# Optimization experiments

Hardware: AMD Instinct MI355X
Metric: run time of the kernel (lower is better)

Reference implementation:

```python
import jax, jax.numpy as jnp
import numpy as np

ALPHA = 0.1
BETA = 0.3
MARGIN = 2.0


def setup_inputs() -> dict:
    key = jax.random.key(0)
    k1, k2 = jax.random.split(key)
    prediction = jax.random.normal(k1, (8, 2048, 512), dtype=jnp.float32)
    target_seg = jax.random.randint(k2, (8, 2048), 0, 16, dtype=jnp.int64)
    return {"prediction": prediction, "target_seg": target_seg}


def _pairwise_sqdist(x):
    # x: [n, L, d] -> squared Euclidean distances [n, L, L] via a GEMM
    sq = jnp.sum(x * x, axis=-1)  # [n, L]
    inner = jnp.einsum('nld,nmd->nlm', x, x)  # [n, L, L]
    d2 = sq[:, :, None] + sq[:, None, :] - 2.0 * inner
    return jnp.maximum(d2, 0.0)


def _safe_sqrt(d2):
    # sqrt with zero (not NaN) gradient at 0, matching torch.cdist behavior
    pos = d2 > 0
    return jnp.where(pos, jnp.sqrt(jnp.where(pos, d2, 1.0)), 0.0)


def reference(prediction, target_seg):
    # y[i,j,k] = 1 if target_seg[i,j] == target_seg[i,k]
    y = (target_seg[:, :, None] == target_seg[:, None, :]).astype(prediction.dtype)
    d2 = _pairwise_sqdist(prediction)
    dist = _safe_sqrt(d2)
    hinge = jnp.maximum(MARGIN - dist, 0.0)
    loss = ALPHA * y * d2 + BETA * (1.0 - y) * hinge * hinge
    return jnp.mean(loss)
```

## Files before the change

### kernel.cpp

```cpp
#include <hip/hip_runtime.h>
#include <math.h>

#define L      2048
#define DDIM   512
#define NBATCH 8
#define BM     128
#define BN     128
#define BK     64
#define NKT    (DDIM / BK)
#define NTILE  (L / BM)
#define NPAIR  (NTILE * (NTILE + 1) / 2)
#define TOTAL_BLOCKS (NBATCH * NPAIR)

#define ALPHA  0.1f
#define BETA   0.3f
#define MARGIN 2.0f

typedef _Float16 f16x8 __attribute__((ext_vector_type(8)));
typedef __attribute__((ext_vector_type(16))) float f32x16;

#define TILE_SH 8192
#define BUFSZ   16384

#define GLOAD_LDS16(g, l) __builtin_amdgcn_global_load_lds(              \
    (const __attribute__((address_space(1))) unsigned int*)(g),          \
    (__attribute__((address_space(3))) unsigned int*)(l), 16, 0, 0)

__global__ __launch_bounds__(256) void conv_kernel(const float* __restrict__ pred,
                                                   _Float16* __restrict__ h,
                                                   float* __restrict__ sq) {
    int w    = threadIdx.x >> 6;
    int lane = threadIdx.x & 63;
    int row  = blockIdx.x * 4 + w;
    const float* p = pred + (size_t)row * DDIM + lane * 8;
    float4 v0 = *(const float4*)(p);
    float4 v1 = *(const float4*)(p + 4);
    float vals[8] = {v0.x, v0.y, v0.z, v0.w, v1.x, v1.y, v1.z, v1.w};
    f16x8 hv;
    float s = 0.0f;
    #pragma unroll
    for (int i = 0; i < 8; ++i) {
        float x = vals[i];
        s = fmaf(x, x, s);
        hv[i] = (_Float16)x;
    }
    *(f16x8*)(h + (size_t)row * DDIM + lane * 8) = hv;
    #pragma unroll
    for (int off = 32; off > 0; off >>= 1) s += __shfl_down(s, off);
    if (lane == 0) sq[row] = s;
}

__global__ __launch_bounds__(256, 2) void loss_kernel(
        const _Float16* __restrict__ h,
        const int*   __restrict__ seg,
        const float* __restrict__ sq,
        double*      __restrict__ partials) {
    __shared__ _Float16 smem[2 * BUFSZ];

    int bid = blockIdx.x;
    int n = bid & 7;
    int p = bid >> 3;
    int tj = 0;
    while (true) {
        int rl2 = NTILE - tj;
        if (p < rl2) break;
        p -= rl2;
        ++tj;
    }
    int tk = tj + p;
    int j0 = tj * BM, k0 = tk * BN;

    int t    = threadIdx.x;
    int w    = t >> 6;
    int lane = t & 63;
    int wr   = w >> 1, wc = w & 1;
    int l31  = lane & 31;
    int hsel = lane >> 5;

    const _Float16* baseH = h + (size_t)n * L * DDIM;

    int rl8 = lane >> 3;
    int lc  = (lane & 7) ^ rl8;
    const _Float16* srcAbase = baseH + (size_t)(j0 + rl8) * DDIM + lc * 8;
    const _Float16* srcBbase = baseH + (size_t)(k0 + rl8) * DDIM + lc * 8;

    f32x16 acc[2][2];
    #pragma unroll
    for (int m = 0; m < 2; ++m)
        #pragma unroll
        for (int nn = 0; nn < 2; ++nn)
            #pragma unroll
            for (int r = 0; r < 16; ++r) acc[m][nn][r] = 0.0f;

    #define STAGE(kt, b)                                                      \
    {                                                                         \
        _Float16* _A = smem + (b) * BUFSZ;                                    \
        _Float16* _B = _A + TILE_SH;                                          \
        _Pragma("unroll")                                                     \
        for (int q = 0; q < 4; ++q) {                                         \
            int inst = w * 4 + q;                                             \
            GLOAD_LDS16(srcAbase + (size_t)(inst * 8) * DDIM + (kt) * BK,     \
                        _A + inst * 512);                                     \
            GLOAD_LDS16(srcBbase + (size_t)(inst * 8) * DDIM + (kt) * BK,     \
                        _B + inst * 512);                                     \
        }                                                                     \
    }

    STAGE(0, 0);
    asm volatile("s_waitcnt vmcnt(0)" ::: "memory");
    __builtin_amdgcn_s_barrier();

    #pragma unroll
    for (int kt = 0; kt < NKT; ++kt) {
        const int cur = kt & 1;
        if (kt + 1 < NKT) STAGE(kt + 1, cur ^ 1);

        const _Float16* A = smem + cur * BUFSZ;
        const _Float16* B = A + TILE_SH;

        #pragma unroll
        for (int ks = 0; ks < 4; ++ks) {
            int c = ks * 2 + hsel;
            f16x8 af[2], bf[2];
            #pragma unroll
            for (int m = 0; m < 2; ++m) {
                int R = wr * 64 + m * 32 + l31;
                af[m] = *(const f16x8*)&A[R * 64 + ((c ^ (R & 7)) << 3)];
            }
            #pragma unroll
            for (int nn = 0; nn < 2; ++nn) {
                int R = wc * 64 + nn * 32 + l31;
                bf[nn] = *(const f16x8*)&B[R * 64 + ((c ^ (R & 7)) << 3)];
            }
            __builtin_amdgcn_s_setprio(1);
            #pragma unroll
            for (int m = 0; m < 2; ++m)
                #pragma unroll
                for (int nn = 0; nn < 2; ++nn)
                    acc[m][nn] = __builtin_amdgcn_mfma_f32_32x32x16_f16(
                        af[m], bf[nn], acc[m][nn], 0, 0, 0);
            __builtin_amdgcn_s_setprio(0);
        }

        asm volatile("s_waitcnt vmcnt(0)" ::: "memory");
        __builtin_amdgcn_s_barrier();
    }

    const int*   segb = seg + n * L;
    const float* sqb  = sq + n * L;

    float lsum = 0.0f;
    #pragma unroll
    for (int nn = 0; nn < 2; ++nn) {
        int k = k0 + wc * 64 + nn * 32 + l31;
        float sqk = sqb[k];
        int   sgk = segb[k];
        #pragma unroll
        for (int m = 0; m < 2; ++m)
            #pragma unroll
            for (int r = 0; r < 16; ++r) {
                int j = j0 + wr * 64 + m * 32 + (r & 3) + 8 * (r >> 2) + 4 * hsel;
                float inner = acc[m][nn][r];
                float d2 = fmaxf(sqb[j] + sqk - 2.0f * inner, 0.0f);
                float v;
                if (segb[j] == sgk) {
                    v = ALPHA * d2;
                } else {
                    float dist = sqrtf(d2);
                    float hg = fmaxf(MARGIN - dist, 0.0f);
                    v = BETA * hg * hg;
                }
                lsum += v;
            }
    }

    double wgt = (tj == tk) ? 1.0 : 2.0;
    __syncthreads();
    double* red = (double*)smem;
    red[t] = (double)lsum * wgt;
    __syncthreads();
    #pragma unroll
    for (int s = 128; s > 0; s >>= 1) {
        if (t < s) red[t] += red[t + s];
        __syncthreads();
    }
    if (t == 0) partials[blockIdx.x] = red[0];
}

__global__ __launch_bounds__(256) void reduce_kernel(const double* __restrict__ partials,
                                                     float* __restrict__ out,
                                                     int nPart, double invCount) {
    __shared__ double red[256];
    int t = threadIdx.x;
    double s = 0.0;
    for (int i = t; i < nPart; i += 256) s += partials[i];
    red[t] = s;
    __syncthreads();
    #pragma unroll
    for (int k = 128; k > 0; k >>= 1) {
        if (t < k) red[t] += red[t + k];
        __syncthreads();
    }
    if (t == 0) out[0] = (float)(red[0] * invCount);
}

extern "C" void kernel_launch(void* const* d_in, const int* in_sizes, int n_in,
                              void* d_out, int out_size, void* d_ws, size_t ws_size,
                              hipStream_t stream) {
    const float* pred = (const float*)d_in[0];
    const int*   seg  = (const int*)d_in[1];
    float* out = (float*)d_out;

    const size_t HALF = (size_t)NBATCH * L * DDIM;
    _Float16* h        = (_Float16*)d_ws;
    float*    sq       = (float*)(h + HALF);
    double*   partials = (double*)(sq + NBATCH * L);

    conv_kernel<<<NBATCH * L / 4, 256, 0, stream>>>(pred, h, sq);
    loss_kernel<<<TOTAL_BLOCKS, 256, 0, stream>>>(h, seg, sq, partials);
    reduce_kernel<<<1, 256, 0, stream>>>(partials, out, TOTAL_BLOCKS,
                                         1.0 / (double)((size_t)NBATCH * L * L));
}
```

Measured before the change: 66.13 us.

## Use four-stage BK=32 LDS ring with prefetch depth two and wave-shuffle reduction

Halves the K-tile to 32 and replaces the double buffer with a four-slot LDS ring. Global-to-LDS loads are issued two stages ahead, and a partial vmcnt wait keeps one stage in flight, so only one barrier per iteration remains. The final block reduction now uses wave shuffles plus a four-entry shared array instead of a shared-memory tree with many barriers. The swizzle width is reduced to match the 32-wide rows, which may raise LDS bank conflicts, and per-iteration overhead doubles because there are twice as many K steps.

```diff
diff --git a/kernel.cpp b/kernel.cpp
--- a/kernel.cpp
+++ b/kernel.cpp
@@ -6,7 +6,7 @@
 #define NBATCH 8
 #define BM     128
 #define BN     128
-#define BK     64
+#define BK     32
 #define NKT    (DDIM / BK)
 #define NTILE  (L / BM)
 #define NPAIR  (NTILE * (NTILE + 1) / 2)
@@ -19,8 +19,8 @@
 typedef _Float16 f16x8 __attribute__((ext_vector_type(8)));
 typedef __attribute__((ext_vector_type(16))) float f32x16;
 
-#define TILE_SH 8192
-#define BUFSZ   16384
+#define TILE_SH 4096
+#define BUFSZ   8192
 
 #define GLOAD_LDS16(g, l) __builtin_amdgcn_global_load_lds(              \
     (const __attribute__((address_space(1))) unsigned int*)(g),          \
@@ -55,7 +55,8 @@
         const int*   __restrict__ seg,
         const float* __restrict__ sq,
         double*      __restrict__ partials) {
-    __shared__ _Float16 smem[2 * BUFSZ];
+    __shared__ _Float16 smem[4 * BUFSZ];
+    __shared__ double wred[4];
 
     int bid = blockIdx.x;
     int n = bid & 7;
@@ -79,10 +80,10 @@
 
     const _Float16* baseH = h + (size_t)n * L * DDIM;
 
-    int rl8 = lane >> 3;
-    int lc  = (lane & 7) ^ rl8;
-    const _Float16* srcAbase = baseH + (size_t)(j0 + rl8) * DDIM + lc * 8;
-    const _Float16* srcBbase = baseH + (size_t)(k0 + rl8) * DDIM + lc * 8;
+    int rl4 = lane >> 2;
+    int lc  = (lane & 3) ^ (rl4 & 3);
+    const _Float16* srcA = baseH + (size_t)(j0 + rl4) * DDIM + lc * 8;
+    const _Float16* srcB = baseH + (size_t)(k0 + rl4) * DDIM + lc * 8;
 
     f32x16 acc[2][2];
     #pragma unroll
@@ -92,45 +93,49 @@
             #pragma unroll
             for (int r = 0; r < 16; ++r) acc[m][nn][r] = 0.0f;
 
-    #define STAGE(kt, b)                                                      \
+    #define STAGE(kt)                                                         \
     {                                                                         \
-        _Float16* _A = smem + (b) * BUFSZ;                                    \
+        _Float16* _A = smem + ((kt) & 3) * BUFSZ;                             \
         _Float16* _B = _A + TILE_SH;                                          \
         _Pragma("unroll")                                                     \
-        for (int q = 0; q < 4; ++q) {                                         \
-            int inst = w * 4 + q;                                             \
-            GLOAD_LDS16(srcAbase + (size_t)(inst * 8) * DDIM + (kt) * BK,     \
+        for (int q = 0; q < 2; ++q) {                                         \
+            int inst = w * 2 + q;                                             \
+            GLOAD_LDS16(srcA + (size_t)(inst * 16) * DDIM + (kt) * BK,        \
                         _A + inst * 512);                                     \
-            GLOAD_LDS16(srcBbase + (size_t)(inst * 8) * DDIM + (kt) * BK,     \
+            GLOAD_LDS16(srcB + (size_t)(inst * 16) * DDIM + (kt) * BK,        \
                         _B + inst * 512);                                     \
         }                                                                     \
     }
 
-    STAGE(0, 0);
-    asm volatile("s_waitcnt vmcnt(0)" ::: "memory");
-    __builtin_amdgcn_s_barrier();
+    STAGE(0);
+    STAGE(1);
 
     #pragma unroll
     for (int kt = 0; kt < NKT; ++kt) {
-        const int cur = kt & 1;
-        if (kt + 1 < NKT) STAGE(kt + 1, cur ^ 1);
-
-        const _Float16* A = smem + cur * BUFSZ;
+        if (kt + 1 < NKT) {
+            asm volatile("s_waitcnt vmcnt(4)" ::: "memory");
+        } else {
+            asm volatile("s_waitcnt vmcnt(0)" ::: "memory");
+        }
+        __builtin_amdgcn_s_barrier();
+        if (kt + 2 < NKT) STAGE(kt + 2);
+
+        const _Float16* A = smem + (kt & 3) * BUFSZ;
         const _Float16* B = A + TILE_SH;
 
         #pragma unroll
-        for (int ks = 0; ks < 4; ++ks) {
+        for (int ks = 0; ks < 2; ++ks) {
             int c = ks * 2 + hsel;
             f16x8 af[2], bf[2];
             #pragma unroll
             for (int m = 0; m < 2; ++m) {
                 int R = wr * 64 + m * 32 + l31;
-                af[m] = *(const f16x8*)&A[R * 64 + ((c ^ (R & 7)) << 3)];
+                af[m] = *(const f16x8*)&A[R * 32 + ((c ^ (R & 3)) << 3)];
             }
             #pragma unroll
             for (int nn = 0; nn < 2; ++nn) {
                 int R = wc * 64 + nn * 32 + l31;
-                bf[nn] = *(const f16x8*)&B[R * 64 + ((c ^ (R & 7)) << 3)];
+                bf[nn] = *(const f16x8*)&B[R * 32 + ((c ^ (R & 3)) << 3)];
             }
             __builtin_amdgcn_s_setprio(1);
             #pragma unroll
@@ -141,9 +146,6 @@
                         af[m], bf[nn], acc[m][nn], 0, 0, 0);
             __builtin_amdgcn_s_setprio(0);
         }
-
-        asm volatile("s_waitcnt vmcnt(0)" ::: "memory");
-        __builtin_amdgcn_s_barrier();
     }
 
     const int*   segb = seg + n * L;
@@ -175,16 +177,13 @@
     }
 
     double wgt = (tj == tk) ? 1.0 : 2.0;
+    double dsum = (double)lsum * wgt;
+    #pragma unroll
+    for (int off = 32; off > 0; off >>= 1)
+        dsum += __shfl_down(dsum, off);
+    if (lane == 0) wred[w] = dsum;
     __syncthreads();
-    double* red = (double*)smem;
-    red[t] = (double)lsum * wgt;
-    __syncthreads();
-    #pragma unroll
-    for (int s = 128; s > 0; s >>= 1) {
-        if (t < s) red[t] += red[t + s];
-        __syncthreads();
-    }
-    if (t == 0) partials[blockIdx.x] = red[0];
+    if (t == 0) partials[bid] = (wred[0] + wred[1]) + (wred[2] + wred[3]);
 }
 
 __global__ __launch_bounds__(256) void reduce_kernel(const double* __restrict__ partials,
```

Measured after the change: 69.89 us. +5.7%, slower.
